# Kernel tuning notes

Hardware: AMD Instinct MI355X
Metric: run time of the kernel (lower is better)

The kernel has to match this reference:

```python
import jax, jax.numpy as jnp
import numpy as np

N, DIM, H, W = 4, 64, 192, 192
K, DIL = 3, 1
STEP = DIL + 1
US = K + DIL * (K - 1)   # effective unfold window = 5
PAD = US // 2
EPS = 1e-5
D4 = DIM // 4


def group_norm(x, gamma, beta, groups=4, eps=EPS):
    n, c = x.shape[0], x.shape[1]
    xg = x.reshape(n, groups, -1)
    m = xg.mean(axis=2, keepdims=True)
    v = xg.var(axis=2, keepdims=True)
    xg = (xg - m) / jnp.sqrt(v + eps)
    xn = xg.reshape(x.shape)
    shp = (1, c) + (1,) * (x.ndim - 2)
    return xn * gamma.reshape(shp) + beta.reshape(shp)


def conv1x1(x, w, b):
    return jnp.einsum('nchw,oc->nohw', x, w) + b.reshape(1, -1, 1, 1)


def dwconv3(x, w, b, dilation):
    c = x.shape[1]
    p = dilation
    y = jax.lax.conv_general_dilated(x, w, (1, 1), [(p, p), (p, p)],
        rhs_dilation=(dilation, dilation), feature_group_count=c,
        dimension_numbers=('NCHW', 'OIHW', 'NCHW'))
    return y + b.reshape(1, -1, 1, 1)


def conv3(x, w, b):
    y = jax.lax.conv_general_dilated(x, w, (1, 1), [(1, 1), (1, 1)],
        dimension_numbers=('NCHW', 'OIHW', 'NCHW'))
    return y + b.reshape(1, -1, 1, 1)


def prelu(x, a):
    return jnp.where(x >= 0, x, a * x)


def forward(x, w_filter, gnf_g, gnf_b,
            lb_w1, lb_b1, lb_a1, lb_dw1, lb_db1,
            lb_w2, lb_b2, lb_a2, lb_dw2, lb_db2,
            lb_w3, lb_b3, lb_a3, lb_dw3, lb_db3,
            lb_w4, lb_b4, lb_a4, lb_w5, lb_b5,
            hb_gn_g, hb_gn_b, hb_w, hb_b,
            fu_w1, fu_b1, fu_gn_g, fu_gn_b, fu_w2, fu_b2):
    n, c, h, w = x.shape
    # dynamic per-channel filter from global average pool (1x1 spatial)
    fp = x.mean(axis=(2, 3))                          # [n, dim]
    fw = fp @ w_filter.T                              # 1x1 conv, no bias -> [n, dim*K*K]
    fw = group_norm(fw[:, :, None, None], gnf_g, gnf_b).reshape(n, DIM, K * K)
    fsm = jax.nn.softmax(fw, axis=2)                  # softmax over the K*K kernel taps
    # masked unfold == gather only the 9 dilated (stride-STEP) taps from reflect-padded x
    xp = jnp.pad(x, ((0, 0), (0, 0), (PAD, PAD), (PAD, PAD)), mode='reflect')
    taps = jnp.stack([xp[:, :, i:i + h, j:j + w]
                      for i in range(0, US, STEP)
                      for j in range(0, US, STEP)], axis=2)   # [n, dim, K*K, h, w]
    low = jnp.einsum('ndkhw,ndk->ndhw', taps, fsm)
    high = x - low
    # low-frequency branch
    y = prelu(conv1x1(low, lb_w1, lb_b1), lb_a1)
    y = dwconv3(y, lb_dw1, lb_db1, 5)
    y = prelu(conv1x1(y, lb_w2, lb_b2), lb_a2)
    y = dwconv3(y, lb_dw2, lb_db2, 1)
    y = prelu(conv1x1(y, lb_w3, lb_b3), lb_a3)
    y = dwconv3(y, lb_dw3, lb_db3, 3)
    y = prelu(conv1x1(y, lb_w4, lb_b4), lb_a4)
    enh_low = conv1x1(y, lb_w5, lb_b5)
    # high-frequency branch (GroupNorm -> LeakyReLU -> 3x3 conv) + residual
    z = group_norm(high, hb_gn_g, hb_gn_b)
    z = jnp.where(z >= 0, z, 0.01 * z)
    enh_high = conv3(z, hb_w, hb_b) + high
    # fusion
    fused = jnp.concatenate([enh_low, enh_high], axis=1)
    o = conv1x1(fused, fu_w1, fu_b1)
    o = group_norm(o, fu_gn_g, fu_gn_b)
    o = jax.nn.gelu(o, approximate=False)
    return conv1x1(o, fu_w2, fu_b2)


def setup_inputs():
    key = jax.random.key(0)
    ks = jax.random.split(key, 16)
    f32 = jnp.float32
    d, d4 = DIM, D4
    rn = lambda k, shape, s=0.05: jax.random.normal(k, shape, dtype=f32) * s
    a = lambda: jnp.array(0.25, f32)   # PReLU init
    return {
        'x': jax.random.normal(ks[0], (N, d, H, W), dtype=f32),
        'w_filter': rn(ks[1], (d * K * K, d)),
        'gnf_g': jnp.ones((d * K * K,), f32), 'gnf_b': jnp.zeros((d * K * K,), f32),
        'lb_w1': rn(ks[2], (d4, d)), 'lb_b1': jnp.zeros((d4,), f32), 'lb_a1': a(),
        'lb_dw1': rn(ks[3], (d4, 1, 3, 3)), 'lb_db1': jnp.zeros((d4,), f32),
        'lb_w2': rn(ks[4], (d4, d4)), 'lb_b2': jnp.zeros((d4,), f32), 'lb_a2': a(),
        'lb_dw2': rn(ks[5], (d4, 1, 3, 3)), 'lb_db2': jnp.zeros((d4,), f32),
        'lb_w3': rn(ks[6], (d4, d4)), 'lb_b3': jnp.zeros((d4,), f32), 'lb_a3': a(),
        'lb_dw3': rn(ks[7], (d4, 1, 3, 3)), 'lb_db3': jnp.zeros((d4,), f32),
        'lb_w4': rn(ks[8], (d4, d4)), 'lb_b4': jnp.zeros((d4,), f32), 'lb_a4': a(),
        'lb_w5': rn(ks[9], (d, d4)), 'lb_b5': jnp.zeros((d,), f32),
        'hb_gn_g': jnp.ones((d,), f32), 'hb_gn_b': jnp.zeros((d,), f32),
        'hb_w': rn(ks[10], (d, d, 3, 3)), 'hb_b': jnp.zeros((d,), f32),
        'fu_w1': rn(ks[11], (2 * d, 2 * d)), 'fu_b1': jnp.zeros((2 * d,), f32),
        'fu_gn_g': jnp.ones((2 * d,), f32), 'fu_gn_b': jnp.zeros((2 * d,), f32),
        'fu_w2': rn(ks[12], (d, 2 * d)), 'fu_b2': jnp.zeros((d,), f32),
    }


def reference(x, w_filter, gnf_g, gnf_b, lb_w1, lb_b1, lb_a1, lb_dw1, lb_db1, lb_w2, lb_b2, lb_a2, lb_dw2, lb_db2, lb_w3, lb_b3, lb_a3, lb_dw3, lb_db3, lb_w4, lb_b4, lb_a4, lb_w5, lb_b5, hb_gn_g, hb_gn_b, hb_w, hb_b, fu_w1, fu_b1, fu_gn_g, fu_gn_b, fu_w2, fu_b2):
    return forward(x, w_filter, gnf_g, gnf_b, lb_w1, lb_b1, lb_a1, lb_dw1, lb_db1, lb_w2, lb_b2, lb_a2, lb_dw2, lb_db2, lb_w3, lb_b3, lb_a3, lb_dw3, lb_db3, lb_w4, lb_b4, lb_a4, lb_w5, lb_b5, hb_gn_g, hb_gn_b, hb_w, hb_b, fu_w1, fu_b1, fu_gn_g, fu_gn_b, fu_w2, fu_b2)
```

## Files before the change

### kernel.cpp

```cpp
#include <hip/hip_runtime.h>
#include <hip/hip_bf16.h>
#include <math.h>

#define Nn 4
#define Cc 64
#define Hh 192
#define Ww 192
#define HW (Hh*Ww)
#define PIXBLK 144

typedef __attribute__((ext_vector_type(4))) float f32x4;
typedef __attribute__((ext_vector_type(8))) short s16x8;

struct __align__(8) US4 { unsigned short x,y,z,w; };

static __device__ __forceinline__ unsigned short f2bf(float v){
    __hip_bfloat16 b = __float2bfloat16(v);
    return *(unsigned short*)&b;
}
static __device__ __forceinline__ float bf2f(unsigned int u){
    return __uint_as_float(u<<16);
}

__global__ void k_gap(const float* __restrict__ x, float* __restrict__ fp){
    int nc = blockIdx.x;
    const float* p = x + (size_t)nc*HW;
    float s = 0.f;
    for(int i=threadIdx.x;i<HW;i+=256) s += p[i];
    for(int o=32;o>0;o>>=1) s += __shfl_down(s,o);
    __shared__ float sm[4];
    int wid = threadIdx.x>>6, ln = threadIdx.x&63;
    if(ln==0) sm[wid]=s;
    __syncthreads();
    if(threadIdx.x==0) fp[nc] = (sm[0]+sm[1]+sm[2]+sm[3]) / (float)HW;
}

__global__ void k_filter(const float* __restrict__ fp, const float* __restrict__ wf,
                         const float* __restrict__ gg, const float* __restrict__ gb,
                         float* __restrict__ fsm){
    int n = blockIdx.x;
    __shared__ float sfp[64];
    __shared__ float sfw[576];
    __shared__ float gstat[8];
    int t = threadIdx.x;
    if(t<64) sfp[t] = fp[n*64+t];
    __syncthreads();
    const float* wr = wf + (size_t)t*64;
    float acc = 0.f;
    #pragma unroll 8
    for(int k=0;k<64;k++) acc += sfp[k]*wr[k];
    sfw[t] = acc;
    __syncthreads();
    if(t<4){
        float s=0.f,s2=0.f;
        for(int i=0;i<144;i++){ float v=sfw[t*144+i]; s+=v; s2+=v*v; }
        float m = s/144.f;
        gstat[t*2]   = m;
        gstat[t*2+1] = s2/144.f - m*m;
    }
    __syncthreads();
    int g = t/144;
    float m = gstat[g*2], var = gstat[g*2+1];
    float z = (acc-m)*rsqrtf(var+1e-5f)*gg[t] + gb[t];
    sfw[t] = z;
    __syncthreads();
    if(t<64){
        float mx = -1e30f;
        for(int j=0;j<9;j++) mx = fmaxf(mx, sfw[t*9+j]);
        float e[9]; float se=0.f;
        for(int j=0;j<9;j++){ e[j]=expf(sfw[t*9+j]-mx); se+=e[j]; }
        float inv = 1.f/se;
        for(int j=0;j<9;j++) fsm[((size_t)n*64+t)*9+j] = e[j]*inv;
    }
}

#define HBS 72
__global__ void __launch_bounds__(256,2)
k_lowhigh(const float* __restrict__ x, const float* __restrict__ fsm,
          const float* __restrict__ w1, const float* __restrict__ b1,
          const float* __restrict__ a1p,
          unsigned short* __restrict__ high, float* __restrict__ y1,
          float* __restrict__ partial){
    int bid = blockIdx.x;
    int n = bid/72, tile = bid%72;
    int h0 = (tile/6)*16, w0 = (tile%6)*32;
    int t = threadIdx.x;
    int r0 = t>>5, wl = t&31;
    __shared__ __align__(16) unsigned short highbuf[512*HBS];
    __shared__ float sf[64*9];
    __shared__ float sw[16*64];
    __shared__ float sb[16];
    __shared__ float redsm[4][8];
    for(int i=t;i<576;i+=256) sf[i] = fsm[(size_t)n*576+i];
    for(int i=t;i<1024;i+=256) sw[i] = w1[i];
    if(t<16) sb[t] = b1[t];
    __syncthreads();
    int rh0[3], rh1[3], rw[3];
    #pragma unroll
    for(int k=0;k<3;k++){
        int a = h0 + r0 + 2*(k-1);     if(a<0) a=-a; if(a>=Hh) a=2*(Hh-1)-a; rh0[k]=a;
        int b = h0 + r0+8 + 2*(k-1);   if(b<0) b=-b; if(b>=Hh) b=2*(Hh-1)-b; rh1[k]=b;
        int c = w0 + wl + 2*(k-1);     if(c<0) c=-c; if(c>=Ww) c=2*(Ww-1)-c; rw[k]=c;
    }
    float accA[16], accB[16];
    #pragma unroll
    for(int o=0;o<16;o++){ accA[o]=0.f; accB[o]=0.f; }
    const float* xb = x + (size_t)n*Cc*HW;
    int p0 = r0*32 + wl, p1 = (r0+8)*32 + wl;
    int wv = t>>6, ln = t&63;
    #pragma unroll 1
    for(int grp=0; grp<4; grp++){
        float sg=0.f, sq=0.f;
        #pragma unroll 1
        for(int sub=0; sub<2; sub++){
            int oct = grp*2 + sub;
            unsigned int hpA[4], hpB[4];
            #pragma unroll
            for(int j=0;j<8;j++){
                int c = oct*8 + j;
                const float* xc = xb + (size_t)c*HW;
                float lowA=0.f, lowB=0.f, ctrA=0.f, ctrB=0.f;
                #pragma unroll
                for(int ki=0;ki<3;ki++){
                    #pragma unroll
                    for(int kj=0;kj<3;kj++){
                        float f = sf[c*9 + ki*3 + kj];
                        float vA = xc[rh0[ki]*Ww + rw[kj]];
                        float vB = xc[rh1[ki]*Ww + rw[kj]];
                        lowA += f*vA; lowB += f*vB;
                        if(ki==1 && kj==1){ ctrA=vA; ctrB=vB; }
                    }
                }
                float hA = ctrA-lowA, hB = ctrB-lowB;
                sg += hA+hB; sq += hA*hA + hB*hB;
                unsigned short a16=f2bf(hA), b16=f2bf(hB);
                if(j&1){ hpA[j>>1] |= ((unsigned int)a16)<<16; hpB[j>>1] |= ((unsigned int)b16)<<16; }
                else   { hpA[j>>1] = a16; hpB[j>>1] = b16; }
                #pragma unroll
                for(int o=0;o<16;o++){
                    float f1w = sw[o*64+c];
                    accA[o] += f1w*lowA; accB[o] += f1w*lowB;
                }
            }
            uint4 pkA; pkA.x=hpA[0]; pkA.y=hpA[1]; pkA.z=hpA[2]; pkA.w=hpA[3];
            uint4 pkB; pkB.x=hpB[0]; pkB.y=hpB[1]; pkB.z=hpB[2]; pkB.w=hpB[3];
            *(uint4*)&highbuf[p0*HBS + oct*8] = pkA;
            *(uint4*)&highbuf[p1*HBS + oct*8] = pkB;
        }
        #pragma unroll
        for(int o=32;o>0;o>>=1){ sg+=__shfl_down(sg,o); sq+=__shfl_down(sq,o); }
        if(ln==0){ redsm[wv][grp*2]=sg; redsm[wv][grp*2+1]=sq; }
    }
    float a1 = *a1p;
    #pragma unroll
    for(int o=0;o<16;o++){
        float vA = accA[o] + sb[o];
        float vB = accB[o] + sb[o];
        vA = vA>=0.f ? vA : a1*vA;
        vB = vB>=0.f ? vB : a1*vB;
        y1[((size_t)n*16 + o)*HW + (h0+r0)*Ww + w0 + wl]   = vA;
        y1[((size_t)n*16 + o)*HW + (h0+r0+8)*Ww + w0 + wl] = vB;
    }
    __syncthreads();
    uint4* gout = (uint4*)(high + (size_t)n*HW*64);
    #pragma unroll
    for(int r=0;r<16;r++){
        int px_l = r*32 + (t>>3);
        uint4 v = *(const uint4*)&highbuf[px_l*HBS + (t&7)*8];
        gout[((size_t)(h0+r)*Ww + w0 + (t>>3))*8 + (t&7)] = v;
    }
    if(t<8) partial[(size_t)bid*8 + t] = redsm[0][t]+redsm[1][t]+redsm[2][t]+redsm[3][t];
}

template<int DILT>
__global__ void k_dw_c(const float* __restrict__ yin,
                       const float* __restrict__ dw, const float* __restrict__ db,
                       const float* __restrict__ wc, const float* __restrict__ bc,
                       const float* __restrict__ ap, float* __restrict__ yout){
    int bid = blockIdx.x;
    int n = bid/PIXBLK;
    int pix = (bid%PIXBLK)*256 + threadIdx.x;
    int h = pix/Ww, w = pix%Ww;
    __shared__ float sdw[16*9];
    __shared__ float swc[16*16];
    __shared__ float sdb[16], sbc[16];
    if(threadIdx.x<144) sdw[threadIdx.x] = dw[threadIdx.x];
    if(threadIdx.x>=144 && threadIdx.x<144+16){ sdb[threadIdx.x-144]=db[threadIdx.x-144]; }
    if(threadIdx.x>=160 && threadIdx.x<160+16){ sbc[threadIdx.x-160]=bc[threadIdx.x-160]; }
    for(int i=threadIdx.x;i<256;i+=256) swc[i]=wc[i];
    __syncthreads();
    float t16[16];
    const float* yb = yin + (size_t)n*16*HW;
    for(int c=0;c<16;c++){
        float s = 0.f;
        #pragma unroll
        for(int u=0;u<3;u++){
            int hh = h + DILT*(u-1);
            if(hh<0 || hh>=Hh) continue;
            #pragma unroll
            for(int v=0;v<3;v++){
                int wwi = w + DILT*(v-1);
                if(wwi<0 || wwi>=Ww) continue;
                s += yb[(size_t)c*HW + hh*Ww + wwi]*sdw[c*9+u*3+v];
            }
        }
        t16[c] = s + sdb[c];
    }
    float a = *ap;
    #pragma unroll
    for(int o=0;o<16;o++){
        float s = sbc[o];
        #pragma unroll
        for(int c=0;c<16;c++) s += swc[o*16+c]*t16[c];
        s = s>=0.f ? s : a*s;
        yout[((size_t)n*16 + o)*HW + pix] = s;
    }
}

__global__ void k_dw3_final(const float* __restrict__ yin,
                            const float* __restrict__ dw, const float* __restrict__ db,
                            const float* __restrict__ w4, const float* __restrict__ b4,
                            const float* __restrict__ a4p,
                            const float* __restrict__ w5, const float* __restrict__ b5,
                            unsigned short* __restrict__ enh_low){
    int bid = blockIdx.x;
    int n = bid/PIXBLK;
    int pix = (bid%PIXBLK)*256 + threadIdx.x;
    int h = pix/Ww, w = pix%Ww;
    __shared__ float sdw[16*9];
    __shared__ float sw4[16*16];
    __shared__ float sw5[64*16];
    __shared__ float sdb[16], sb4[16], sb5[64];
    if(threadIdx.x<144) sdw[threadIdx.x]=dw[threadIdx.x];
    if(threadIdx.x<16){ sdb[threadIdx.x]=db[threadIdx.x]; sb4[threadIdx.x]=b4[threadIdx.x]; }
    if(threadIdx.x<64) sb5[threadIdx.x]=b5[threadIdx.x];
    for(int i=threadIdx.x;i<256;i+=256) sw4[i]=w4[i];
    for(int i=threadIdx.x;i<1024;i+=256) sw5[i]=w5[i];
    __syncthreads();
    float t16[16];
    const float* yb = yin + (size_t)n*16*HW;
    for(int c=0;c<16;c++){
        float s=0.f;
        #pragma unroll
        for(int u=0;u<3;u++){
            int hh = h + 3*(u-1);
            if(hh<0||hh>=Hh) continue;
            #pragma unroll
            for(int v=0;v<3;v++){
                int wwi = w + 3*(v-1);
                if(wwi<0||wwi>=Ww) continue;
                s += yb[(size_t)c*HW + hh*Ww + wwi]*sdw[c*9+u*3+v];
            }
        }
        t16[c] = s + sdb[c];
    }
    float a = *a4p;
    float y4[16];
    #pragma unroll
    for(int o=0;o<16;o++){
        float s = sb4[o];
        #pragma unroll
        for(int c=0;c<16;c++) s += sw4[o*16+c]*t16[c];
        y4[o] = s>=0.f ? s : a*s;
    }
    unsigned short* dst = enh_low + ((size_t)n*HW + pix)*64;
    #pragma unroll
    for(int ob=0;ob<64;ob+=4){
        unsigned short tmp[4];
        #pragma unroll
        for(int j=0;j<4;j++){
            int o=ob+j;
            float s = sb5[o];
            #pragma unroll
            for(int c=0;c<16;c++) s += sw5[o*16+c]*y4[c];
            tmp[j]=f2bf(s);
        }
        US4 pk; pk.x=tmp[0]; pk.y=tmp[1]; pk.z=tmp[2]; pk.w=tmp[3];
        *(US4*)&dst[ob] = pk;
    }
}

__global__ void k_redstats(const float* __restrict__ partial, float* __restrict__ st, int nblk){
    int b = blockIdx.x;
    int n = b>>2, gl = b&3;
    int tid = threadIdx.x;
    float a0=0.f, a1=0.f;
    for(int pt=tid; pt<nblk; pt+=256){
        size_t base = (size_t)(n*nblk+pt)*8 + gl*2;
        a0 += partial[base];
        a1 += partial[base+1];
    }
    #pragma unroll
    for(int o=32;o>0;o>>=1){ a0+=__shfl_down(a0,o); a1+=__shfl_down(a1,o); }
    __shared__ float sm[8];
    int wv=tid>>6, ln=tid&63;
    if(ln==0){ sm[wv*2]=a0; sm[wv*2+1]=a1; }
    __syncthreads();
    if(tid==0){
        st[b*32+0] = sm[0]+sm[2]+sm[4]+sm[6];
        st[b*32+1] = sm[1]+sm[3]+sm[5]+sm[7];
    }
}

__global__ void k_wprep2(const float* __restrict__ hw, const float* __restrict__ fw1,
                         const float* __restrict__ fw2,
                         unsigned short* __restrict__ g_wt,
                         unsigned short* __restrict__ g_wfu1,
                         unsigned short* __restrict__ g_wfu2){
    int idx = blockIdx.x*256 + threadIdx.x;
    if(idx<36864){
        int c = idx & 63;
        int o = (idx>>6) & 15;
        int t = (idx>>10) % 9;
        int og = idx / 9216;
        float v = hw[(size_t)(((og*16+o)*64)+c)*9 + t];
        g_wt[(size_t)og*9216 + (t*16+o)*64 + (c ^ ((o&7)<<3))] = f2bf(v);
    } else if(idx<53248){
        int i = idx-36864;
        int o = i>>7, c = i&127;
        g_wfu1[o*128 + (c ^ ((o&15)<<3))] = f2bf(fw1[i]);
    } else {
        int i = idx-53248;
        int o = i>>7, c = i&127;
        g_wfu2[o*128 + (c ^ ((o&15)<<3))] = f2bf(fw2[i]);
    }
}

__global__ void __launch_bounds__(256,2)
k_conv3m(const unsigned short* __restrict__ high, const float* __restrict__ st,
         const float* __restrict__ gng, const float* __restrict__ gnb,
         const unsigned short* __restrict__ g_wt, const float* __restrict__ hb,
         unsigned short* __restrict__ enh_high){
    int bid = blockIdx.x;
    int tile = bid % 144;
    int og   = (bid/144) & 3;
    int n    = bid / 576;
    int tr0 = (tile/12)*16, tc0 = (tile%12)*16;
    __shared__ __align__(16) unsigned short z_lds[324*64];
    __shared__ __align__(16) unsigned short wt_lds[9*16*64];
    __shared__ float ssc[64], sbi[64];
    int tid = threadIdx.x;
    {
        const uint4* src = (const uint4*)(g_wt + (size_t)og*9216);
        uint4* dst = (uint4*)wt_lds;
        for(int i=tid;i<1152;i+=256) dst[i]=src[i];
    }
    if(tid<64){
        int c=tid, g=n*4+(c>>4);
        float cnt=16.f*(float)HW;
        float m=st[g*32]/cnt, var=st[g*32+1]/cnt-m*m;
        float sc=gng[c]*rsqrtf(var+1e-5f);
        ssc[c]=sc; sbi[c]=gnb[c]-m*sc;
    }
    __syncthreads();
    const uint4* hpm = (const uint4*)(high + (size_t)n*HW*64);
    for(int e=tid;e<2592;e+=256){
        int hpx = e>>3, q = e&7;
        int hr = hpx/18, hc = hpx - hr*18;
        int gr = tr0+hr-1, gc = tc0+hc-1;
        uint4 w; w.x=0; w.y=0; w.z=0; w.w=0;
        if(gr>=0 && gr<Hh && gc>=0 && gc<Ww){
            uint4 v = hpm[(size_t)(gr*Ww+gc)*8 + q];
            unsigned int vv[4]={v.x,v.y,v.z,v.w};
            #pragma unroll
            for(int j=0;j<4;j++){
                int c = q*8 + 2*j;
                float f0 = bf2f(vv[j]&0xffffu)*ssc[c]   + sbi[c];
                float f1 = bf2f(vv[j]>>16)   *ssc[c+1] + sbi[c+1];
                f0 = f0>=0.f ? f0 : 0.01f*f0;
                f1 = f1>=0.f ? f1 : 0.01f*f1;
                vv[j] = (unsigned int)f2bf(f0) | ((unsigned int)f2bf(f1)<<16);
            }
            w.x=vv[0]; w.y=vv[1]; w.z=vv[2]; w.w=vv[3];
        }
        *(uint4*)&z_lds[hpx*64 + ((q*8) ^ ((hpx&7)<<3))] = w;
    }
    __syncthreads();
    int wv = tid>>6, ln = tid&63;
    int col = ln&15, kq = ln>>4;
    f32x4 acc[4] = {{0.f,0.f,0.f,0.f},{0.f,0.f,0.f,0.f},{0.f,0.f,0.f,0.f},{0.f,0.f,0.f,0.f}};
    #pragma unroll
    for(int t=0;t<9;t++){
        int dr = t/3 - 1, dc = t%3 - 1;
        #pragma unroll
        for(int kb=0;kb<2;kb++){
            int k0 = kb*32 + kq*8;
            const s16x8 afr = *(const s16x8*)&wt_lds[(t*16+col)*64 + (k0 ^ ((col&7)<<3))];
            #pragma unroll
            for(int rf=0;rf<4;rf++){
                int r = wv*4 + rf;
                int hpx = (r+1+dr)*18 + (col+1+dc);
                const s16x8 bfr = *(const s16x8*)&z_lds[hpx*64 + (k0 ^ ((hpx&7)<<3))];
                acc[rf] = __builtin_amdgcn_mfma_f32_16x16x32_bf16(afr, bfr, acc[rf], 0, 0, 0);
            }
        }
    }
    const unsigned short* hres = high + (size_t)n*HW*64;
    #pragma unroll
    for(int rf=0;rf<4;rf++){
        int r = wv*4 + rf;
        int gpx = (tr0+r)*Ww + (tc0+col);
        US4 rv = *(const US4*)&hres[(size_t)gpx*64 + og*16 + kq*4];
        unsigned short tmp[4];
        float rvf[4] = {bf2f(rv.x), bf2f(rv.y), bf2f(rv.z), bf2f(rv.w)};
        #pragma unroll
        for(int reg=0;reg<4;reg++){
            int oc = og*16 + kq*4 + reg;
            tmp[reg] = f2bf(acc[rf][reg] + hb[oc] + rvf[reg]);
        }
        US4 pk; pk.x=tmp[0]; pk.y=tmp[1]; pk.z=tmp[2]; pk.w=tmp[3];
        *(US4*)&enh_high[((size_t)n*HW + gpx)*64 + og*16 + kq*4] = pk;
    }
}

__global__ void __launch_bounds__(256,2)
k_fu1m(const unsigned short* __restrict__ el, const unsigned short* __restrict__ eh,
       const unsigned short* __restrict__ wA, const float* __restrict__ b,
       unsigned short* __restrict__ o1, float* __restrict__ partial){
    int bid = blockIdx.x;
    int n = bid/288, pt = bid%288;
    int px0 = pt*128;
    __shared__ __align__(16) unsigned short sA[128*128];
    __shared__ __align__(16) unsigned short sB[128*128];
    __shared__ float sb[128];
    __shared__ float redsm[16];
    int tid = threadIdx.x;
    {
        const uint4* s=(const uint4*)wA; uint4* d=(uint4*)sA;
        for(int i=tid;i<2048;i+=256) d[i]=s[i];
    }
    if(tid<128) sb[tid]=b[tid];
    {
        const uint4* se=(const uint4*)(el + ((size_t)n*HW+px0)*64);
        const uint4* sh=(const uint4*)(eh + ((size_t)n*HW+px0)*64);
        for(int i=tid;i<2048;i+=256){
            int px=i>>4, q=i&15;
            uint4 v = (q<8)? se[px*8+q] : sh[px*8+(q-8)];
            int c0 = q*8;
            *(uint4*)&sB[px*128 + (c0 ^ ((px&15)<<3))] = v;
        }
    }
    __syncthreads();
    int wv=tid>>6, ln=tid&63;
    int wm=wv>>1, wn=wv&1;
    int col=ln&15, kq=ln>>4;
    f32x4 acc[4][4];
    #pragma unroll
    for(int m=0;m<4;m++)
        #pragma unroll
        for(int nf=0;nf<4;nf++) acc[m][nf]=(f32x4){0.f,0.f,0.f,0.f};
    #pragma unroll
    for(int kb=0;kb<4;kb++){
        int k0 = kb*32 + kq*8;
        s16x8 a[4], bf[4];
        #pragma unroll
        for(int m=0;m<4;m++)
            a[m] = *(const s16x8*)&sA[(wm*64+m*16+col)*128 + (k0 ^ (col<<3))];
        #pragma unroll
        for(int nf=0;nf<4;nf++)
            bf[nf] = *(const s16x8*)&sB[(wn*64+nf*16+col)*128 + (k0 ^ (col<<3))];
        #pragma unroll
        for(int m=0;m<4;m++)
            #pragma unroll
            for(int nf=0;nf<4;nf++)
                acc[m][nf] = __builtin_amdgcn_mfma_f32_16x16x32_bf16(a[m], bf[nf], acc[m][nf], 0,0,0);
    }
    float sg0=0.f,sq0=0.f,sg1=0.f,sq1=0.f;
    #pragma unroll
    for(int m=0;m<4;m++){
        int oc0 = wm*64 + m*16 + kq*4;
        #pragma unroll
        for(int nf=0;nf<4;nf++){
            int px = wn*64 + nf*16 + col;
            unsigned short tmp[4];
            #pragma unroll
            for(int reg=0;reg<4;reg++){
                float v = acc[m][nf][reg] + sb[oc0+reg];
                if(m<2){ sg0+=v; sq0+=v*v; } else { sg1+=v; sq1+=v*v; }
                tmp[reg]=f2bf(v);
            }
            US4 pk; pk.x=tmp[0]; pk.y=tmp[1]; pk.z=tmp[2]; pk.w=tmp[3];
            *(US4*)&o1[((size_t)n*HW + px0 + px)*128 + oc0] = pk;
        }
    }
    #pragma unroll
    for(int o=32;o>0;o>>=1){
        sg0+=__shfl_down(sg0,o); sq0+=__shfl_down(sq0,o);
        sg1+=__shfl_down(sg1,o); sq1+=__shfl_down(sq1,o);
    }
    if(ln==0){ redsm[wv*4+0]=sg0; redsm[wv*4+1]=sq0; redsm[wv*4+2]=sg1; redsm[wv*4+3]=sq1; }
    __syncthreads();
    if(tid<8){
        int gl = tid>>1, comp = tid&1;
        int wbase = (gl>>1)*2;
        int off = (gl&1)*2 + comp;
        partial[(size_t)bid*8 + tid] = redsm[wbase*4+off] + redsm[(wbase+1)*4+off];
    }
}

__global__ void __launch_bounds__(256,2)
k_fu2m(const unsigned short* __restrict__ o1, const float* __restrict__ st,
       const float* __restrict__ gg, const float* __restrict__ gb,
       const unsigned short* __restrict__ wA, const float* __restrict__ b2,
       float* __restrict__ out){
    int bid = blockIdx.x;
    int n = bid/288, pt = bid%288;
    int px0 = pt*128;
    __shared__ __align__(16) unsigned short sA[64*128];
    __shared__ __align__(16) unsigned short sB[128*128];
    __shared__ float ssc[128], sbi[128], sb2[64];
    int tid = threadIdx.x;
    {
        const uint4* s=(const uint4*)wA; uint4* d=(uint4*)sA;
        for(int i=tid;i<1024;i+=256) d[i]=s[i];
    }
    if(tid<128){
        int c=tid, g=n*4+(c>>5);
        float cnt = 32.f*(float)HW;
        float m = st[g*32]/cnt;
        float var = st[g*32+1]/cnt - m*m;
        float sc = gg[c]*rsqrtf(var+1e-5f);
        ssc[c]=sc; sbi[c]=gb[c]-m*sc;
    }
    if(tid<64) sb2[tid]=b2[tid];
    __syncthreads();
    {
        const uint4* so=(const uint4*)(o1 + ((size_t)n*HW+px0)*128);
        for(int i=tid;i<2048;i+=256){
            int px=i>>4, q=i&15;
            int c0 = q*8;
            uint4 v = so[px*16+q];
            unsigned int vals[4] = {v.x,v.y,v.z,v.w};
            #pragma unroll
            for(int j=0;j<4;j++){
                int c = c0 + 2*j;
                float f0 = bf2f(vals[j]&0xffffu)*ssc[c]   + sbi[c];
                float f1 = bf2f(vals[j]>>16)   *ssc[c+1] + sbi[c+1];
                f0 = 0.5f*f0*(1.f+erff(f0*0.70710678118654752f));
                f1 = 0.5f*f1*(1.f+erff(f1*0.70710678118654752f));
                vals[j] = (unsigned int)f2bf(f0) | ((unsigned int)f2bf(f1)<<16);
            }
            uint4 w; w.x=vals[0]; w.y=vals[1]; w.z=vals[2]; w.w=vals[3];
            *(uint4*)&sB[px*128 + (c0 ^ ((px&15)<<3))] = w;
        }
    }
    __syncthreads();
    int wv=tid>>6, ln=tid&63;
    int col=ln&15, kq=ln>>4;
    f32x4 acc[4][2];
    #pragma unroll
    for(int m=0;m<4;m++){ acc[m][0]=(f32x4){0,0,0,0}; acc[m][1]=(f32x4){0,0,0,0}; }
    #pragma unroll
    for(int kb=0;kb<4;kb++){
        int k0 = kb*32 + kq*8;
        s16x8 a[4], bf[2];
        #pragma unroll
        for(int m=0;m<4;m++)
            a[m] = *(const s16x8*)&sA[(m*16+col)*128 + (k0 ^ (col<<3))];
        #pragma unroll
        for(int nf=0;nf<2;nf++)
            bf[nf] = *(const s16x8*)&sB[(wv*32+nf*16+col)*128 + (k0 ^ (col<<3))];
        #pragma unroll
        for(int m=0;m<4;m++)
            #pragma unroll
            for(int nf=0;nf<2;nf++)
                acc[m][nf] = __builtin_amdgcn_mfma_f32_16x16x32_bf16(a[m], bf[nf], acc[m][nf], 0,0,0);
    }
    #pragma unroll
    for(int m=0;m<4;m++){
        int oc0 = m*16 + kq*4;
        #pragma unroll
        for(int nf=0;nf<2;nf++){
            int px = px0 + wv*32 + nf*16 + col;
            #pragma unroll
            for(int reg=0;reg<4;reg++){
                int oc = oc0+reg;
                out[((size_t)n*64+oc)*HW + px] = acc[m][nf][reg] + sb2[oc];
            }
        }
    }
}

extern "C" void kernel_launch(void* const* d_in, const int* in_sizes, int n_in,
                              void* d_out, int out_size, void* d_ws, size_t ws_size,
                              hipStream_t stream) {
    const float* x        = (const float*)d_in[0];
    const float* w_filter = (const float*)d_in[1];
    const float* gnf_g    = (const float*)d_in[2];
    const float* gnf_b    = (const float*)d_in[3];
    const float* lb_w1    = (const float*)d_in[4];
    const float* lb_b1    = (const float*)d_in[5];
    const float* lb_a1    = (const float*)d_in[6];
    const float* lb_dw1   = (const float*)d_in[7];
    const float* lb_db1   = (const float*)d_in[8];
    const float* lb_w2    = (const float*)d_in[9];
    const float* lb_b2    = (const float*)d_in[10];
    const float* lb_a2    = (const float*)d_in[11];
    const float* lb_dw2   = (const float*)d_in[12];
    const float* lb_db2   = (const float*)d_in[13];
    const float* lb_w3    = (const float*)d_in[14];
    const float* lb_b3    = (const float*)d_in[15];
    const float* lb_a3    = (const float*)d_in[16];
    const float* lb_dw3   = (const float*)d_in[17];
    const float* lb_db3   = (const float*)d_in[18];
    const float* lb_w4    = (const float*)d_in[19];
    const float* lb_b4    = (const float*)d_in[20];
    const float* lb_a4    = (const float*)d_in[21];
    const float* lb_w5    = (const float*)d_in[22];
    const float* lb_b5    = (const float*)d_in[23];
    const float* hb_gn_g  = (const float*)d_in[24];
    const float* hb_gn_b  = (const float*)d_in[25];
    const float* hb_w     = (const float*)d_in[26];
    const float* hb_b     = (const float*)d_in[27];
    const float* fu_w1    = (const float*)d_in[28];
    const float* fu_b1    = (const float*)d_in[29];
    const float* fu_gn_g  = (const float*)d_in[30];
    const float* fu_gn_b  = (const float*)d_in[31];
    const float* fu_w2    = (const float*)d_in[32];
    const float* fu_b2    = (const float*)d_in[33];
    float* out = (float*)d_out;

    const size_t O1B = (size_t)Nn*HW*128*2;
    const size_t EB  = (size_t)Nn*HW*64*2;
    const size_t YB  = (size_t)Nn*16*HW*4;
    char* Wb = (char*)d_ws;
    unsigned short* o1       = (unsigned short*)Wb;
    unsigned short* high     = (unsigned short*)Wb;
    unsigned short* enh_low  = (unsigned short*)(Wb + O1B);
    unsigned short* enh_high = (unsigned short*)(Wb + O1B + EB);
    float* y1                = (float*)(Wb + O1B + 2*EB);
    float* y2                = (float*)(Wb + O1B + 2*EB + YB);
    unsigned short* g_wt     = (unsigned short*)(Wb + O1B + 2*EB + 2*YB);
    unsigned short* g_wfu1   = g_wt + 36864;
    unsigned short* g_wfu2   = g_wfu1 + 16384;
    float* fp      = (float*)(g_wfu2 + 8192);
    float* fsm     = fp + 256;
    float* st_hb   = fsm + 2304;
    float* st_o1   = st_hb + 512;
    float* part_hb = st_o1 + 512;
    float* part_o1 = part_hb + 2304;

    k_wprep2<<<240, 256, 0, stream>>>(hb_w, fu_w1, fu_w2, g_wt, g_wfu1, g_wfu2);
    k_gap<<<Nn*Cc, 256, 0, stream>>>(x, fp);
    k_filter<<<Nn, 576, 0, stream>>>(fp, w_filter, gnf_g, gnf_b, fsm);
    k_lowhigh<<<Nn*72, 256, 0, stream>>>(x, fsm, lb_w1, lb_b1, lb_a1, high, y1, part_hb);
    k_redstats<<<16, 256, 0, stream>>>(part_hb, st_hb, 72);
    k_dw_c<5><<<Nn*PIXBLK, 256, 0, stream>>>(y1, lb_dw1, lb_db1, lb_w2, lb_b2, lb_a2, y2);
    k_dw_c<1><<<Nn*PIXBLK, 256, 0, stream>>>(y2, lb_dw2, lb_db2, lb_w3, lb_b3, lb_a3, y1);
    k_dw3_final<<<Nn*PIXBLK, 256, 0, stream>>>(y1, lb_dw3, lb_db3, lb_w4, lb_b4, lb_a4,
                                               lb_w5, lb_b5, enh_low);
    k_conv3m<<<Nn*4*144, 256, 0, stream>>>(high, st_hb, hb_gn_g, hb_gn_b, g_wt, hb_b, enh_high);
    k_fu1m<<<Nn*288, 256, 0, stream>>>(enh_low, enh_high, g_wfu1, fu_b1, o1, part_o1);
    k_redstats<<<16, 256, 0, stream>>>(part_o1, st_o1, 288);
    k_fu2m<<<Nn*288, 256, 0, stream>>>(o1, st_o1, fu_gn_g, fu_gn_b, g_wfu2, fu_b2, out);
}
```

Before: 536.6 us.

## Merge prep kernels, shrink lowhigh tiles, compute all output groups per conv3 block

Folds the weight-prep and global-average-pool kernels into one launch and vectorises the pooling loads. The low/high kernel now handles 16x16 tiles with one pixel per thread, doubling the block count and raising the occupancy hint. The 3x3 conv kernel computes all four output-channel groups per block, so the normalised input tile is staged into LDS once instead of four times. Weights are now read directly from global memory, unswizzled, and the conv launch moves ahead of the depthwise chain. The cost is more accumulator registers per thread in the conv and uncached global weight fetches inside the MFMA loop.

```diff
diff --git a/kernel.cpp b/kernel.cpp
--- a/kernel.cpp
+++ b/kernel.cpp
@@ -22,17 +22,41 @@
     return __uint_as_float(u<<16);
 }
 
-__global__ void k_gap(const float* __restrict__ x, float* __restrict__ fp){
-    int nc = blockIdx.x;
-    const float* p = x + (size_t)nc*HW;
-    float s = 0.f;
-    for(int i=threadIdx.x;i<HW;i+=256) s += p[i];
-    for(int o=32;o>0;o>>=1) s += __shfl_down(s,o);
+__global__ void k_prep(const float* __restrict__ hw, const float* __restrict__ fw1,
+                       const float* __restrict__ fw2, const float* __restrict__ x,
+                       unsigned short* __restrict__ g_wt,
+                       unsigned short* __restrict__ g_wfu1,
+                       unsigned short* __restrict__ g_wfu2,
+                       float* __restrict__ fp){
+    int b = blockIdx.x;
     __shared__ float sm[4];
-    int wid = threadIdx.x>>6, ln = threadIdx.x&63;
-    if(ln==0) sm[wid]=s;
-    __syncthreads();
-    if(threadIdx.x==0) fp[nc] = (sm[0]+sm[1]+sm[2]+sm[3]) / (float)HW;
+    if(b < 240){
+        int idx = b*256 + threadIdx.x;
+        if(idx<36864){
+            int og = idx/9216, r = idx%9216;
+            int t = r/1024, r2 = r%1024;
+            int o = r2>>6, c = r2&63;
+            g_wt[idx] = f2bf(hw[(size_t)(((og*16+o)*64)+c)*9 + t]);
+        } else if(idx<53248){
+            int i = idx-36864;
+            int o = i>>7, c = i&127;
+            g_wfu1[o*128 + (c ^ ((o&15)<<3))] = f2bf(fw1[i]);
+        } else {
+            int i = idx-53248;
+            int o = i>>7, c = i&127;
+            g_wfu2[o*128 + (c ^ ((o&15)<<3))] = f2bf(fw2[i]);
+        }
+    } else {
+        int nc = b-240;
+        const float4* p = (const float4*)(x + (size_t)nc*HW);
+        float s = 0.f;
+        for(int i=threadIdx.x;i<HW/4;i+=256){ float4 v=p[i]; s += v.x+v.y+v.z+v.w; }
+        for(int o=32;o>0;o>>=1) s += __shfl_down(s,o);
+        int wid = threadIdx.x>>6, ln = threadIdx.x&63;
+        if(ln==0) sm[wid]=s;
+        __syncthreads();
+        if(threadIdx.x==0) fp[nc] = (sm[0]+sm[1]+sm[2]+sm[3]) / (float)HW;
+    }
 }
 
 __global__ void k_filter(const float* __restrict__ fp, const float* __restrict__ wf,
@@ -74,39 +98,37 @@
     }
 }
 
-#define HBS 72
-__global__ void __launch_bounds__(256,2)
+#define HBS 88
+__global__ void __launch_bounds__(256,3)
 k_lowhigh(const float* __restrict__ x, const float* __restrict__ fsm,
           const float* __restrict__ w1, const float* __restrict__ b1,
           const float* __restrict__ a1p,
           unsigned short* __restrict__ high, float* __restrict__ y1,
           float* __restrict__ partial){
     int bid = blockIdx.x;
-    int n = bid/72, tile = bid%72;
-    int h0 = (tile/6)*16, w0 = (tile%6)*32;
+    int n = bid/144, tile = bid%144;
+    int h0 = (tile/12)*16, w0 = (tile%12)*16;
     int t = threadIdx.x;
-    int r0 = t>>5, wl = t&31;
-    __shared__ __align__(16) unsigned short highbuf[512*HBS];
-    __shared__ float sf[64*9];
-    __shared__ float sw[16*64];
+    int r0 = t>>4, wl = t&15;
+    __shared__ __align__(16) unsigned short highbuf[256*HBS];
+    __shared__ float sf[576];
+    __shared__ float sw[1024];
     __shared__ float sb[16];
     __shared__ float redsm[4][8];
     for(int i=t;i<576;i+=256) sf[i] = fsm[(size_t)n*576+i];
     for(int i=t;i<1024;i+=256) sw[i] = w1[i];
     if(t<16) sb[t] = b1[t];
     __syncthreads();
-    int rh0[3], rh1[3], rw[3];
+    int rh[3], rw[3];
     #pragma unroll
     for(int k=0;k<3;k++){
-        int a = h0 + r0 + 2*(k-1);     if(a<0) a=-a; if(a>=Hh) a=2*(Hh-1)-a; rh0[k]=a;
-        int b = h0 + r0+8 + 2*(k-1);   if(b<0) b=-b; if(b>=Hh) b=2*(Hh-1)-b; rh1[k]=b;
-        int c = w0 + wl + 2*(k-1);     if(c<0) c=-c; if(c>=Ww) c=2*(Ww-1)-c; rw[k]=c;
-    }
-    float accA[16], accB[16];
-    #pragma unroll
-    for(int o=0;o<16;o++){ accA[o]=0.f; accB[o]=0.f; }
+        int a = h0 + r0 + 2*(k-1); if(a<0) a=-a; if(a>=Hh) a=2*(Hh-1)-a; rh[k]=a;
+        int c = w0 + wl + 2*(k-1); if(c<0) c=-c; if(c>=Ww) c=2*(Ww-1)-c; rw[k]=c;
+    }
+    float acc[16];
+    #pragma unroll
+    for(int o=0;o<16;o++) acc[o]=0.f;
     const float* xb = x + (size_t)n*Cc*HW;
-    int p0 = r0*32 + wl, p1 = (r0+8)*32 + wl;
     int wv = t>>6, ln = t&63;
     #pragma unroll 1
     for(int grp=0; grp<4; grp++){
@@ -114,38 +136,30 @@
         #pragma unroll 1
         for(int sub=0; sub<2; sub++){
             int oct = grp*2 + sub;
-            unsigned int hpA[4], hpB[4];
+            unsigned int hp[4];
             #pragma unroll
             for(int j=0;j<8;j++){
                 int c = oct*8 + j;
                 const float* xc = xb + (size_t)c*HW;
-                float lowA=0.f, lowB=0.f, ctrA=0.f, ctrB=0.f;
+                float low=0.f, ctr=0.f;
                 #pragma unroll
                 for(int ki=0;ki<3;ki++){
                     #pragma unroll
                     for(int kj=0;kj<3;kj++){
-                        float f = sf[c*9 + ki*3 + kj];
-                        float vA = xc[rh0[ki]*Ww + rw[kj]];
-                        float vB = xc[rh1[ki]*Ww + rw[kj]];
-                        lowA += f*vA; lowB += f*vB;
-                        if(ki==1 && kj==1){ ctrA=vA; ctrB=vB; }
+                        float v = xc[rh[ki]*Ww + rw[kj]];
+                        low += sf[c*9 + ki*3 + kj]*v;
+                        if(ki==1 && kj==1) ctr = v;
                     }
                 }
-                float hA = ctrA-lowA, hB = ctrB-lowB;
-                sg += hA+hB; sq += hA*hA + hB*hB;
-                unsigned short a16=f2bf(hA), b16=f2bf(hB);
-                if(j&1){ hpA[j>>1] |= ((unsigned int)a16)<<16; hpB[j>>1] |= ((unsigned int)b16)<<16; }
-                else   { hpA[j>>1] = a16; hpB[j>>1] = b16; }
+                float hv = ctr-low;
+                sg += hv; sq += hv*hv;
+                unsigned short h16 = f2bf(hv);
+                if(j&1) hp[j>>1] |= ((unsigned int)h16)<<16; else hp[j>>1] = h16;
                 #pragma unroll
-                for(int o=0;o<16;o++){
-                    float f1w = sw[o*64+c];
-                    accA[o] += f1w*lowA; accB[o] += f1w*lowB;
-                }
-            }
-            uint4 pkA; pkA.x=hpA[0]; pkA.y=hpA[1]; pkA.z=hpA[2]; pkA.w=hpA[3];
-            uint4 pkB; pkB.x=hpB[0]; pkB.y=hpB[1]; pkB.z=hpB[2]; pkB.w=hpB[3];
-            *(uint4*)&highbuf[p0*HBS + oct*8] = pkA;
-            *(uint4*)&highbuf[p1*HBS + oct*8] = pkB;
+                for(int o=0;o<16;o++) acc[o] += sw[o*64+c]*low;
+            }
+            uint4 pk; pk.x=hp[0]; pk.y=hp[1]; pk.z=hp[2]; pk.w=hp[3];
+            *(uint4*)&highbuf[t*HBS + oct*8] = pk;
         }
         #pragma unroll
         for(int o=32;o>0;o>>=1){ sg+=__shfl_down(sg,o); sq+=__shfl_down(sq,o); }
@@ -154,20 +168,18 @@
     float a1 = *a1p;
     #pragma unroll
     for(int o=0;o<16;o++){
-        float vA = accA[o] + sb[o];
-        float vB = accB[o] + sb[o];
-        vA = vA>=0.f ? vA : a1*vA;
-        vB = vB>=0.f ? vB : a1*vB;
-        y1[((size_t)n*16 + o)*HW + (h0+r0)*Ww + w0 + wl]   = vA;
-        y1[((size_t)n*16 + o)*HW + (h0+r0+8)*Ww + w0 + wl] = vB;
+        float v = acc[o] + sb[o];
+        v = v>=0.f ? v : a1*v;
+        y1[((size_t)n*16 + o)*HW + (h0+r0)*Ww + w0 + wl] = v;
     }
     __syncthreads();
     uint4* gout = (uint4*)(high + (size_t)n*HW*64);
     #pragma unroll
-    for(int r=0;r<16;r++){
-        int px_l = r*32 + (t>>3);
-        uint4 v = *(const uint4*)&highbuf[px_l*HBS + (t&7)*8];
-        gout[((size_t)(h0+r)*Ww + w0 + (t>>3))*8 + (t&7)] = v;
+    for(int it=0;it<8;it++){
+        int i = it*256 + t;
+        int px = i>>3, sl = i&7;
+        uint4 v = *(const uint4*)&highbuf[px*HBS + sl*8];
+        gout[((size_t)(h0+(px>>4))*Ww + w0 + (px&15))*8 + sl] = v;
     }
     if(t<8) partial[(size_t)bid*8 + t] = redsm[0][t]+redsm[1][t]+redsm[2][t]+redsm[3][t];
 }
@@ -302,55 +314,24 @@
     }
 }
 
-__global__ void k_wprep2(const float* __restrict__ hw, const float* __restrict__ fw1,
-                         const float* __restrict__ fw2,
-                         unsigned short* __restrict__ g_wt,
-                         unsigned short* __restrict__ g_wfu1,
-                         unsigned short* __restrict__ g_wfu2){
-    int idx = blockIdx.x*256 + threadIdx.x;
-    if(idx<36864){
-        int c = idx & 63;
-        int o = (idx>>6) & 15;
-        int t = (idx>>10) % 9;
-        int og = idx / 9216;
-        float v = hw[(size_t)(((og*16+o)*64)+c)*9 + t];
-        g_wt[(size_t)og*9216 + (t*16+o)*64 + (c ^ ((o&7)<<3))] = f2bf(v);
-    } else if(idx<53248){
-        int i = idx-36864;
-        int o = i>>7, c = i&127;
-        g_wfu1[o*128 + (c ^ ((o&15)<<3))] = f2bf(fw1[i]);
-    } else {
-        int i = idx-53248;
-        int o = i>>7, c = i&127;
-        g_wfu2[o*128 + (c ^ ((o&15)<<3))] = f2bf(fw2[i]);
-    }
-}
-
-__global__ void __launch_bounds__(256,2)
+__global__ void __launch_bounds__(256,3)
 k_conv3m(const unsigned short* __restrict__ high, const float* __restrict__ st,
          const float* __restrict__ gng, const float* __restrict__ gnb,
          const unsigned short* __restrict__ g_wt, const float* __restrict__ hb,
          unsigned short* __restrict__ enh_high){
     int bid = blockIdx.x;
-    int tile = bid % 144;
-    int og   = (bid/144) & 3;
-    int n    = bid / 576;
+    int n = bid/144, tile = bid%144;
     int tr0 = (tile/12)*16, tc0 = (tile%12)*16;
     __shared__ __align__(16) unsigned short z_lds[324*64];
-    __shared__ __align__(16) unsigned short wt_lds[9*16*64];
-    __shared__ float ssc[64], sbi[64];
+    __shared__ float ssc[64], sbi[64], sbias[64];
     int tid = threadIdx.x;
-    {
-        const uint4* src = (const uint4*)(g_wt + (size_t)og*9216);
-        uint4* dst = (uint4*)wt_lds;
-        for(int i=tid;i<1152;i+=256) dst[i]=src[i];
-    }
     if(tid<64){
         int c=tid, g=n*4+(c>>4);
         float cnt=16.f*(float)HW;
         float m=st[g*32]/cnt, var=st[g*32+1]/cnt-m*m;
         float sc=gng[c]*rsqrtf(var+1e-5f);
         ssc[c]=sc; sbi[c]=gnb[c]-m*sc;
+        sbias[c]=hb[c];
     }
     __syncthreads();
     const uint4* hpm = (const uint4*)(high + (size_t)n*HW*64);
@@ -378,20 +359,29 @@
     __syncthreads();
     int wv = tid>>6, ln = tid&63;
     int col = ln&15, kq = ln>>4;
-    f32x4 acc[4] = {{0.f,0.f,0.f,0.f},{0.f,0.f,0.f,0.f},{0.f,0.f,0.f,0.f},{0.f,0.f,0.f,0.f}};
+    f32x4 acc[4][4];
+    #pragma unroll
+    for(int og=0;og<4;og++)
+        #pragma unroll
+        for(int rf=0;rf<4;rf++) acc[og][rf]=(f32x4){0.f,0.f,0.f,0.f};
     #pragma unroll
     for(int t=0;t<9;t++){
         int dr = t/3 - 1, dc = t%3 - 1;
         #pragma unroll
         for(int kb=0;kb<2;kb++){
             int k0 = kb*32 + kq*8;
-            const s16x8 afr = *(const s16x8*)&wt_lds[(t*16+col)*64 + (k0 ^ ((col&7)<<3))];
+            s16x8 afr[4];
+            #pragma unroll
+            for(int og=0;og<4;og++)
+                afr[og] = *(const s16x8*)&g_wt[(size_t)(((og*9+t)*16+col)*64) + k0];
             #pragma unroll
             for(int rf=0;rf<4;rf++){
                 int r = wv*4 + rf;
                 int hpx = (r+1+dr)*18 + (col+1+dc);
                 const s16x8 bfr = *(const s16x8*)&z_lds[hpx*64 + (k0 ^ ((hpx&7)<<3))];
-                acc[rf] = __builtin_amdgcn_mfma_f32_16x16x32_bf16(afr, bfr, acc[rf], 0, 0, 0);
+                #pragma unroll
+                for(int og=0;og<4;og++)
+                    acc[og][rf] = __builtin_amdgcn_mfma_f32_16x16x32_bf16(afr[og], bfr, acc[og][rf], 0, 0, 0);
             }
         }
     }
@@ -400,16 +390,19 @@
     for(int rf=0;rf<4;rf++){
         int r = wv*4 + rf;
         int gpx = (tr0+r)*Ww + (tc0+col);
-        US4 rv = *(const US4*)&hres[(size_t)gpx*64 + og*16 + kq*4];
-        unsigned short tmp[4];
-        float rvf[4] = {bf2f(rv.x), bf2f(rv.y), bf2f(rv.z), bf2f(rv.w)};
-        #pragma unroll
-        for(int reg=0;reg<4;reg++){
-            int oc = og*16 + kq*4 + reg;
-            tmp[reg] = f2bf(acc[rf][reg] + hb[oc] + rvf[reg]);
-        }
-        US4 pk; pk.x=tmp[0]; pk.y=tmp[1]; pk.z=tmp[2]; pk.w=tmp[3];
-        *(US4*)&enh_high[((size_t)n*HW + gpx)*64 + og*16 + kq*4] = pk;
+        #pragma unroll
+        for(int og=0;og<4;og++){
+            US4 rv = *(const US4*)&hres[(size_t)gpx*64 + og*16 + kq*4];
+            float rvf[4] = {bf2f(rv.x), bf2f(rv.y), bf2f(rv.z), bf2f(rv.w)};
+            unsigned short tmp[4];
+            #pragma unroll
+            for(int reg=0;reg<4;reg++){
+                int oc = og*16 + kq*4 + reg;
+                tmp[reg] = f2bf(acc[og][rf][reg] + sbias[oc] + rvf[reg]);
+            }
+            US4 pk; pk.x=tmp[0]; pk.y=tmp[1]; pk.z=tmp[2]; pk.w=tmp[3];
+            *(US4*)&enh_high[((size_t)n*HW + gpx)*64 + og*16 + kq*4] = pk;
+        }
     }
 }
 
@@ -638,18 +631,17 @@
     float* st_hb   = fsm + 2304;
     float* st_o1   = st_hb + 512;
     float* part_hb = st_o1 + 512;
-    float* part_o1 = part_hb + 2304;
-
-    k_wprep2<<<240, 256, 0, stream>>>(hb_w, fu_w1, fu_w2, g_wt, g_wfu1, g_wfu2);
-    k_gap<<<Nn*Cc, 256, 0, stream>>>(x, fp);
+    float* part_o1 = part_hb + 4608;
+
+    k_prep<<<496, 256, 0, stream>>>(hb_w, fu_w1, fu_w2, x, g_wt, g_wfu1, g_wfu2, fp);
     k_filter<<<Nn, 576, 0, stream>>>(fp, w_filter, gnf_g, gnf_b, fsm);
-    k_lowhigh<<<Nn*72, 256, 0, stream>>>(x, fsm, lb_w1, lb_b1, lb_a1, high, y1, part_hb);
-    k_redstats<<<16, 256, 0, stream>>>(part_hb, st_hb, 72);
+    k_lowhigh<<<Nn*144, 256, 0, stream>>>(x, fsm, lb_w1, lb_b1, lb_a1, high, y1, part_hb);
+    k_redstats<<<16, 256, 0, stream>>>(part_hb, st_hb, 144);
+    k_conv3m<<<Nn*144, 256, 0, stream>>>(high, st_hb, hb_gn_g, hb_gn_b, g_wt, hb_b, enh_high);
     k_dw_c<5><<<Nn*PIXBLK, 256, 0, stream>>>(y1, lb_dw1, lb_db1, lb_w2, lb_b2, lb_a2, y2);
     k_dw_c<1><<<Nn*PIXBLK, 256, 0, stream>>>(y2, lb_dw2, lb_db2, lb_w3, lb_b3, lb_a3, y1);
     k_dw3_final<<<Nn*PIXBLK, 256, 0, stream>>>(y1, lb_dw3, lb_db3, lb_w4, lb_b4, lb_a4,
                                                lb_w5, lb_b5, enh_low);
-    k_conv3m<<<Nn*4*144, 256, 0, stream>>>(high, st_hb, hb_gn_g, hb_gn_b, g_wt, hb_b, enh_high);
     k_fu1m<<<Nn*288, 256, 0, stream>>>(enh_low, enh_high, g_wfu1, fu_b1, o1, part_o1);
     k_redstats<<<16, 256, 0, stream>>>(part_o1, st_o1, 288);
     k_fu2m<<<Nn*288, 256, 0, stream>>>(o1, st_o1, fu_gn_g, fu_gn_b, g_wfu2, fu_b2, out);
```

Result: faster. 506.9 us (-5.5%).
